# Kernel tuning notes

Measured on AMD Instinct MI355X. Metric: run time of the kernel, lower is better.

Reference implementation:

```python
import jax, jax.numpy as jnp
import numpy as np

SCALING = 32.0 / 16.0  # lora_alpha / lora_rank


def setup_inputs() -> dict:
    key = jax.random.key(0)
    ks = jax.random.split(key, 6)
    B_, S, D, O, E, R = 4, 2048, 4096, 4096, 8, 16
    x = jax.random.normal(ks[0], (B_, S, D), dtype=jnp.float32)
    W_base = jax.random.normal(ks[1], (O, D), dtype=jnp.float32) * (D ** -0.5)
    b_base = jax.random.normal(ks[2], (O,), dtype=jnp.float32) * 0.01
    W_gate = jax.random.normal(ks[3], (E, D), dtype=jnp.float32) * (D ** -0.5)
    A = jax.random.normal(ks[4], (E, R, D), dtype=jnp.float32) * (D ** -0.5)
    B = jax.random.normal(ks[5], (O, R), dtype=jnp.float32)[None] * (R ** -0.5)
    B = jnp.broadcast_to(B, (E, O, R)) * jnp.linspace(0.5, 1.5, E)[:, None, None]
    return {"x": x, "W_base": W_base, "b_base": b_base, "W_gate": W_gate,
            "A": A, "B": B, "top_k": 2}


def reference(x, W_base, b_base, W_gate, A, B, top_k):
    D = x.shape[-1]
    O = W_base.shape[0]
    E = W_gate.shape[0]
    xf = x.reshape(-1, D)                      # [N, D] flattened tokens
    N = xf.shape[0]

    # base linear
    base = jnp.einsum('nd,od->no', xf, W_base) + b_base          # [N, O]

    # gating: softmax then top-k, renormalize selected weights
    gate_logits = jax.nn.softmax(xf @ W_gate.T, axis=-1)          # [N, E]
    w, sel = jax.lax.top_k(gate_logits, top_k)                    # [N, k]
    w = w / jnp.sum(w, axis=-1, keepdims=True)

    # dense per-(token, expert) weight; non-selected experts get 0,
    # equivalent to the scatter-add combine in the original code.
    w_dense = jnp.zeros((N, E), dtype=x.dtype).at[
        jnp.arange(N)[:, None], sel].set(w)                       # [N, E]

    # LoRA expert compute: down-proj for every expert (rank is small),
    # weight, then up-proj and combine across experts.
    h = jnp.einsum('nd,erd->ner', xf, A)                          # [N, E, R]
    hw = h * w_dense[:, :, None]                                  # [N, E, R]
    moe = jnp.einsum('ner,eor->no', hw, B) * SCALING              # [N, O]

    out = (base + moe).reshape(x.shape[:-1] + (O,))
    return out
```

## Files before the change

### kernel.cpp

```cpp
#include <hip/hip_runtime.h>
#include <stdint.h>

typedef unsigned short u16;
typedef float f32x4 __attribute__((ext_vector_type(4)));
typedef short bf16x8 __attribute__((ext_vector_type(8)));

static __device__ __forceinline__ u16 f2bf(float f) {
  union { float f; unsigned u; } a; a.f = f;
  unsigned r = a.u + 0x7fffu + ((a.u >> 16) & 1u);
  return (u16)(r >> 16);
}

static __device__ __forceinline__ void gld16(const void* g, void* l) {
  __builtin_amdgcn_global_load_lds(
      (const __attribute__((address_space(1))) void*)(uintptr_t)g,
      (__attribute__((address_space(3))) void*)(uintptr_t)l,
      16, 0, 0);
}

__global__ __launch_bounds__(256, 4) void fused_pre(
    const float* __restrict__ x, const float* __restrict__ Wg,
    const float* __restrict__ Wb, const float* __restrict__ B,
    const float* __restrict__ A,
    u16* __restrict__ Xaug, u16* __restrict__ Waug, u16* __restrict__ a2,
    float* __restrict__ wsc) {
  const int bid = blockIdx.x;
  const int t = threadIdx.x;
  if (bid < 512) {
    const int lane = t & 63;
    const int wv = t >> 6;
    const int n0 = bid * 16 + wv * 4;
    const float4* g4 = (const float4*)Wg;
    float acc[4][8] = {};
#pragma unroll 2
    for (int ii = 0; ii < 16; ++ii) {
      const int i = ii * 64 + lane;
      float4 xv[4];
#pragma unroll
      for (int tok = 0; tok < 4; ++tok) {
        xv[tok] = *(const float4*)(x + (size_t)(n0 + tok) * 4096 + i * 4);
        ushort4 o;
        o.x = f2bf(xv[tok].x); o.y = f2bf(xv[tok].y);
        o.z = f2bf(xv[tok].z); o.w = f2bf(xv[tok].w);
        *(ushort4*)(Xaug + (size_t)(n0 + tok) * 4224 + i * 4) = o;
      }
#pragma unroll
      for (int e = 0; e < 8; ++e) {
        float4 w4 = g4[e * 1024 + i];
#pragma unroll
        for (int tok = 0; tok < 4; ++tok)
          acc[tok][e] += xv[tok].x * w4.x + xv[tok].y * w4.y +
                         xv[tok].z * w4.z + xv[tok].w * w4.w;
      }
    }
#pragma unroll
    for (int tok = 0; tok < 4; ++tok) {
#pragma unroll
      for (int e = 0; e < 8; ++e) {
#pragma unroll
        for (int off = 32; off > 0; off >>= 1)
          acc[tok][e] += __shfl_xor(acc[tok][e], off);
      }
      int i1 = 0; float m1 = acc[tok][0];
#pragma unroll
      for (int e = 1; e < 8; ++e) if (acc[tok][e] > m1) { m1 = acc[tok][e]; i1 = e; }
      int i2 = -1; float m2 = -3.4e38f;
#pragma unroll
      for (int e = 0; e < 8; ++e)
        if (e != i1 && acc[tok][e] > m2) { m2 = acc[tok][e]; i2 = e; }
      float w1 = 1.0f / (1.0f + expf(m2 - m1));
      float w2 = 1.0f - w1;
      if (lane < 8)
        wsc[(size_t)(n0 + tok) * 8 + lane] =
            (lane == i1) ? w1 : ((lane == i2) ? w2 : 0.0f);
    }
  } else if (bid < 2560) {
    const int total = 4096 * 1056;
    for (int v = (bid - 512) * 256 + t; v < total; v += 2048 * 256) {
      const int o = v / 1056;
      const int c = (v - o * 1056) * 4;
      ushort4 out;
      if (c < 4096) {
        float4 w = *(const float4*)(Wb + (size_t)o * 4096 + c);
        out.x = f2bf(w.x); out.y = f2bf(w.y); out.z = f2bf(w.z); out.w = f2bf(w.w);
      } else {
        const int er = c - 4096;
        const int e = er >> 4;
        const int r = er & 15;
        const float* bp = B + ((size_t)e * 4096 + o) * 16 + r;
        out.x = f2bf(bp[0] * 2.0f); out.y = f2bf(bp[1] * 2.0f);
        out.z = f2bf(bp[2] * 2.0f); out.w = f2bf(bp[3] * 2.0f);
      }
      *(ushort4*)(Waug + (size_t)o * 4224 + c) = out;
    }
  } else {
    const int i = (bid - 2560) * 256 + t;
    const size_t e = (size_t)i * 4;
    float4 v = *(const float4*)(A + e);
    ushort4 o;
    o.x = f2bf(v.x); o.y = f2bf(v.y); o.z = f2bf(v.z); o.w = f2bf(v.w);
    *(ushort4*)(a2 + e) = o;
  }
}

__global__ __launch_bounds__(256) void lora_hw(
    const u16* __restrict__ Xa, const u16* __restrict__ A2,
    const float* __restrict__ wsc, u16* __restrict__ Xaug) {
  __shared__ __align__(1024) char lds[40960];
  const int t = threadIdx.x;
  const int lane = t & 63;
  const int w = t >> 6;
  const int l15 = lane & 15, lhi = lane >> 4;
  const int brow = blockIdx.x * 32;

  const int sb = (lane << 4) ^ (lane & 32);
  const int srow = sb >> 6;
  const int scol = (sb & 63) >> 1;

  const u16* pA = Xa + (size_t)(brow + (w >> 1) * 16 + srow) * 4224 + (w & 1) * 32 + scol;
  const u16* pB[4];
#pragma unroll
  for (int s = 0; s < 4; ++s) {
    const int idx = w * 4 + s;
    pB[s] = A2 + (size_t)((idx >> 1) * 16 + srow) * 4096 + (idx & 1) * 32 + scol;
  }
  const int dA = w << 10;
  const int dB = 4096 + (w << 12);
  const int innerL = ((l15 << 6) + (lhi << 4)) ^ ((l15 & 8) << 2);

  f32x4 acc[2][2] = {};

  gld16(pA, lds + dA);
#pragma unroll
  for (int s = 0; s < 4; ++s) gld16(pB[s], lds + dB + (s << 10));

  for (int j = 0; j < 64; ++j) {
    const int buf = (j & 1) * 20480;
    const int obuf = buf ^ 20480;
    if (j < 63) {
      const int k1 = (j + 1) * 64;
      gld16(pA + k1, lds + obuf + dA);
#pragma unroll
      for (int s = 0; s < 4; ++s) gld16(pB[s] + k1, lds + obuf + dB + (s << 10));
      asm volatile("s_waitcnt vmcnt(5)" ::: "memory");
    } else {
      asm volatile("s_waitcnt vmcnt(0)" ::: "memory");
    }
    __syncthreads();
    bf16x8 av[2][2], bv[2][2];
#pragma unroll
    for (int m = 0; m < 2; ++m)
#pragma unroll
      for (int kk = 0; kk < 2; ++kk)
        av[m][kk] = *(const bf16x8*)(lds + buf + ((m * 2 + kk) << 10) + innerL);
#pragma unroll
    for (int n = 0; n < 2; ++n)
#pragma unroll
      for (int kk = 0; kk < 2; ++kk)
        bv[n][kk] = *(const bf16x8*)(lds + buf + 4096 + (((w * 2 + n) * 2 + kk) << 10) + innerL);
#pragma unroll
    for (int kk = 0; kk < 2; ++kk)
#pragma unroll
      for (int m = 0; m < 2; ++m)
#pragma unroll
        for (int n = 0; n < 2; ++n)
          acc[m][n] = __builtin_amdgcn_mfma_f32_16x16x32_bf16(av[m][kk], bv[n][kk], acc[m][n], 0, 0, 0);
    __syncthreads();
  }
#pragma unroll
  for (int m = 0; m < 2; ++m) {
    const int rbase = brow + m * 16 + lhi * 4;
#pragma unroll
    for (int n = 0; n < 2; ++n) {
      const int col = w * 32 + n * 16 + l15;
#pragma unroll
      for (int j = 0; j < 4; ++j) {
        const int row = rbase + j;
        const float g = wsc[(size_t)row * 8 + (col >> 4)];
        Xaug[(size_t)row * 4224 + 4096 + col] = f2bf(acc[m][n][j] * g);
      }
    }
  }
}

#define BAR do { asm volatile("" ::: "memory"); __builtin_amdgcn_s_barrier(); asm volatile("" ::: "memory"); } while (0)

#define RDA(BUF, MH)                                                            \
  { _Pragma("unroll") for (int mm = 0; mm < 4; ++mm)                            \
    _Pragma("unroll") for (int kk = 0; kk < 2; ++kk)                            \
      av[mm][kk] = *(const bf16x8*)(lds + (BUF) + fbA + ((((MH) * 4 + mm) * 2 + kk) << 10)); }

#define RDB(BUF, NH)                                                            \
  { _Pragma("unroll") for (int nn = 0; nn < 2; ++nn)                            \
    _Pragma("unroll") for (int kk = 0; kk < 2; ++kk)                            \
      bv[(NH) * 2 + nn][kk] = *(const bf16x8*)(lds + (BUF) + fbB + ((((NH) * 2 + nn) * 2 + kk) << 10)); }

#define MFMAQ(MH, NH)                                                           \
  { __builtin_amdgcn_s_setprio(1);                                              \
    _Pragma("unroll") for (int kk = 0; kk < 2; ++kk)                            \
    _Pragma("unroll") for (int mm = 0; mm < 4; ++mm)                            \
    _Pragma("unroll") for (int nn = 0; nn < 2; ++nn)                            \
      acc[(MH) * 4 + mm][(NH) * 2 + nn] = __builtin_amdgcn_mfma_f32_16x16x32_bf16( \
          av[mm][kk], bv[(NH) * 2 + nn][kk], acc[(MH) * 4 + mm][(NH) * 2 + nn], 0, 0, 0); \
    __builtin_amdgcn_s_setprio(0); }

__global__ __launch_bounds__(512, 2) void gemm8p(
    const u16* __restrict__ Ag, const u16* __restrict__ Bg,
    const float* __restrict__ bias, float* __restrict__ C,
    int lda, int ldb, int ldc, int K) {
  __shared__ __align__(1024) char lds[131072];
  const int t = threadIdx.x;
  const int lane = t & 63;
  const int w = t >> 6;
  const int wr = w >> 2, wc = w & 3;
  const int l15 = lane & 15, lhi = lane >> 4;

  const int bid = blockIdx.x;
  const int g = bid >> 3;
  const int tile_m = (bid & 7) * 4 + (g & 3);
  const int tile_n = g >> 2;
  const int brow = tile_m << 8;
  const int bcol = tile_n << 8;

  const int sb = (lane << 4) ^ (lane & 32);
  const int srow = sb >> 6;
  const int scol = (sb & 63) >> 1;

  const u16* pA[4]; const u16* pB[4];
#pragma unroll
  for (int s = 0; s < 4; ++s) {
    const int idx = w * 4 + s;
    const int rg = idx >> 1, cs = idx & 1;
    pA[s] = Ag + (size_t)(brow + rg * 16 + srow) * lda + cs * 32 + scol;
    pB[s] = Bg + (size_t)(bcol + rg * 16 + srow) * ldb + cs * 32 + scol;
  }
  const int ldsA = w << 12;
  const int ldsB = 32768 + (w << 12);

  const int innerL = ((l15 << 6) + (lhi << 4)) ^ ((l15 & 8) << 2);
  const int fbA = (wr << 14) + innerL;
  const int fbB = 32768 + (wc << 13) + innerL;

  f32x4 acc[8][4] = {};
  bf16x8 av[4][2], bv[4][2];

  const int NT = K >> 6;

#pragma unroll
  for (int s = 0; s < 4; ++s) gld16(pA[s], lds + ldsA + (s << 10));
#pragma unroll
  for (int s = 0; s < 4; ++s) gld16(pB[s], lds + ldsB + (s << 10));
#pragma unroll
  for (int s = 0; s < 4; ++s) gld16(pB[s] + 64, lds + 65536 + ldsB + (s << 10));
#pragma unroll
  for (int s = 0; s < 4; ++s) { pA[s] += 64; pB[s] += 128; }
  asm volatile("s_waitcnt vmcnt(4)" ::: "memory");
  BAR;
  RDA(0, 0); RDB(0, 0);

  for (int j = 0; j < NT; ++j) {
    const int buf  = (j & 1) << 16;
    const int obuf = buf ^ 65536;
    const bool stA = (j + 1 < NT);
    const bool stB = (j + 2 < NT);
    if (stA) { gld16(pA[0], lds + obuf + ldsA);
               gld16(pA[1], lds + obuf + ldsA + 1024); }
    MFMAQ(0, 0);
    RDB(buf, 1);
    BAR;
    if (stA) { gld16(pA[2], lds + obuf + ldsA + 2048);
               gld16(pA[3], lds + obuf + ldsA + 3072); }
    MFMAQ(0, 1);
    RDA(buf, 1);
    BAR;
    if (stB) { gld16(pB[0], lds + buf + ldsB);
               gld16(pB[1], lds + buf + ldsB + 1024); }
    MFMAQ(1, 1);
    BAR;
    if (stB) { gld16(pB[2], lds + buf + ldsB + 2048);
               gld16(pB[3], lds + buf + ldsB + 3072); }
    if (j < NT - 2)       { asm volatile("s_waitcnt vmcnt(4)" ::: "memory"); }
    else if (j == NT - 2) { asm volatile("s_waitcnt vmcnt(0)" ::: "memory"); }
    BAR;
    MFMAQ(1, 0);
    if (stA) { RDA(obuf, 0); RDB(obuf, 0); }
#pragma unroll
    for (int s = 0; s < 4; ++s) { pA[s] += 64; pB[s] += 64; }
  }

#pragma unroll
  for (int m = 0; m < 8; ++m) {
    const int row0 = brow + wr * 128 + m * 16 + lhi * 4;
#pragma unroll
    for (int n = 0; n < 4; ++n) {
      const int col = bcol + wc * 64 + n * 16 + l15;
      const float b2 = bias[col];
#pragma unroll
      for (int jj = 0; jj < 4; ++jj)
        C[(size_t)(row0 + jj) * ldc + col] = acc[m][n][jj] + b2;
    }
  }
}

extern "C" void kernel_launch(void* const* d_in, const int* in_sizes, int n_in,
                              void* d_out, int out_size, void* d_ws, size_t ws_size,
                              hipStream_t stream) {
  const float* x  = (const float*)d_in[0];
  const float* Wb = (const float*)d_in[1];
  const float* bb = (const float*)d_in[2];
  const float* Wg = (const float*)d_in[3];
  const float* A  = (const float*)d_in[4];
  const float* B  = (const float*)d_in[5];
  float* out = (float*)d_out;

  char* ws = (char*)d_ws;
  u16*   Xaug = (u16*)ws;
  u16*   Waug = (u16*)(ws + 69206016);
  u16*   a2   = (u16*)(ws + 69206016 + 34603008);
  float* wsc  = (float*)(ws + 69206016 + 34603008 + 1048576);

  fused_pre<<<3072, 256, 0, stream>>>(x, Wg, Wb, B, A, Xaug, Waug, a2, wsc);

  lora_hw<<<256, 256, 0, stream>>>(Xaug, a2, wsc, Xaug);

  gemm8p<<<512, 512, 0, stream>>>(Xaug, Waug, bb, out, 4224, 4224, 4096, 4224);
}
```

Measured before the change: 331.3 us.

## Restructure GEMM main loop into half-tile staged ping-pong with interleaved wave ownership

Reworks the bf16 GEMM so that each 256x256 tile is split into halves of 128 rows. Each wave now owns interleaved 64x32 sub-blocks across both halves instead of one contiguous 128x64 block. The main loop is unrolled by two K-steps with explicit ping-pong buffers, and global-to-LDS loads are staged per half between barrier-bracketed MFMA quadrants. The intent is finer-grained overlap of loads with MFMA work and lower LDS read pressure, at the cost of many more barriers per iteration and an assumption that the K-tile count is even.

```diff
diff --git a/kernel.cpp b/kernel.cpp
--- a/kernel.cpp
+++ b/kernel.cpp
@@ -185,23 +185,38 @@
 
 #define BAR do { asm volatile("" ::: "memory"); __builtin_amdgcn_s_barrier(); asm volatile("" ::: "memory"); } while (0)
 
-#define RDA(BUF, MH)                                                            \
+#define STG_A(KT, H, DB) do {                                                   \
+    gld16(pAst + (size_t)(H) * 128 * lda + (size_t)(KT) * 64,                   \
+          lds + (DB) + (H) * 16384 + dstOff);                                   \
+    gld16(pAst + (size_t)((H) * 128 + 64) * lda + (size_t)(KT) * 64,            \
+          lds + (DB) + (H) * 16384 + dstOff + 8192);                            \
+  } while (0)
+#define STG_B(KT, H, DB) do {                                                   \
+    gld16(pBst + (size_t)(H) * 128 * ldb + (size_t)(KT) * 64,                   \
+          lds + (DB) + 32768 + (H) * 16384 + dstOff);                           \
+    gld16(pBst + (size_t)((H) * 128 + 64) * ldb + (size_t)(KT) * 64,            \
+          lds + (DB) + 32768 + (H) * 16384 + dstOff + 8192);                    \
+  } while (0)
+
+#define RDA8(DB, MH)                                                            \
   { _Pragma("unroll") for (int mm = 0; mm < 4; ++mm)                            \
     _Pragma("unroll") for (int kk = 0; kk < 2; ++kk)                            \
-      av[mm][kk] = *(const bf16x8*)(lds + (BUF) + fbA + ((((MH) * 4 + mm) * 2 + kk) << 10)); }
-
-#define RDB(BUF, NH)                                                            \
+      av[mm][kk] = *(const bf16x8*)(lds + (DB) + (MH) * 16384 +                 \
+                    (((wr * 4 + mm) * 2 + kk) << 10) + innerL); }
+
+#define RDB4(DB, NH, BV)                                                        \
   { _Pragma("unroll") for (int nn = 0; nn < 2; ++nn)                            \
     _Pragma("unroll") for (int kk = 0; kk < 2; ++kk)                            \
-      bv[(NH) * 2 + nn][kk] = *(const bf16x8*)(lds + (BUF) + fbB + ((((NH) * 2 + nn) * 2 + kk) << 10)); }
-
-#define MFMAQ(MH, NH)                                                           \
+      BV[nn][kk] = *(const bf16x8*)(lds + (DB) + 32768 + (NH) * 16384 +         \
+                    (((wc * 2 + nn) * 2 + kk) << 10) + innerL); }
+
+#define MQ(MH, NH, BV)                                                          \
   { __builtin_amdgcn_s_setprio(1);                                              \
     _Pragma("unroll") for (int kk = 0; kk < 2; ++kk)                            \
     _Pragma("unroll") for (int mm = 0; mm < 4; ++mm)                            \
     _Pragma("unroll") for (int nn = 0; nn < 2; ++nn)                            \
       acc[(MH) * 4 + mm][(NH) * 2 + nn] = __builtin_amdgcn_mfma_f32_16x16x32_bf16( \
-          av[mm][kk], bv[(NH) * 2 + nn][kk], acc[(MH) * 4 + mm][(NH) * 2 + nn], 0, 0, 0); \
+          av[mm][kk], BV[nn][kk], acc[(MH) * 4 + mm][(NH) * 2 + nn], 0, 0, 0);  \
     __builtin_amdgcn_s_setprio(0); }
 
 __global__ __launch_bounds__(512, 2) void gemm8p(
@@ -223,81 +238,66 @@
   const int bcol = tile_n << 8;
 
   const int sb = (lane << 4) ^ (lane & 32);
-  const int srow = sb >> 6;
-  const int scol = (sb & 63) >> 1;
-
-  const u16* pA[4]; const u16* pB[4];
-#pragma unroll
-  for (int s = 0; s < 4; ++s) {
-    const int idx = w * 4 + s;
-    const int rg = idx >> 1, cs = idx & 1;
-    pA[s] = Ag + (size_t)(brow + rg * 16 + srow) * lda + cs * 32 + scol;
-    pB[s] = Bg + (size_t)(bcol + rg * 16 + srow) * ldb + cs * 32 + scol;
-  }
-  const int ldsA = w << 12;
-  const int ldsB = 32768 + (w << 12);
+  const int r0 = (w >> 1) * 16 + (sb >> 6);
+  const int c0 = (w & 1) * 32 + ((sb & 63) >> 1);
+  const u16* pAst = Ag + (size_t)(brow + r0) * lda + c0;
+  const u16* pBst = Bg + (size_t)(bcol + r0) * ldb + c0;
+  const int dstOff = w << 10;
 
   const int innerL = ((l15 << 6) + (lhi << 4)) ^ ((l15 & 8) << 2);
-  const int fbA = (wr << 14) + innerL;
-  const int fbB = 32768 + (wc << 13) + innerL;
 
   f32x4 acc[8][4] = {};
-  bf16x8 av[4][2], bv[4][2];
+  bf16x8 av[4][2], bv[2][2], bv2[2][2];
 
   const int NT = K >> 6;
-
-#pragma unroll
-  for (int s = 0; s < 4; ++s) gld16(pA[s], lds + ldsA + (s << 10));
-#pragma unroll
-  for (int s = 0; s < 4; ++s) gld16(pB[s], lds + ldsB + (s << 10));
-#pragma unroll
-  for (int s = 0; s < 4; ++s) gld16(pB[s] + 64, lds + 65536 + ldsB + (s << 10));
-#pragma unroll
-  for (int s = 0; s < 4; ++s) { pA[s] += 64; pB[s] += 128; }
+  const int NIT = NT >> 1;
+
+  STG_A(0, 0, 0); STG_A(0, 1, 0); STG_B(0, 0, 0); STG_B(0, 1, 0);
+  STG_B(1, 0, 65536); STG_A(1, 0, 65536);
   asm volatile("s_waitcnt vmcnt(4)" ::: "memory");
   BAR;
-  RDA(0, 0); RDB(0, 0);
-
-  for (int j = 0; j < NT; ++j) {
-    const int buf  = (j & 1) << 16;
-    const int obuf = buf ^ 65536;
-    const bool stA = (j + 1 < NT);
-    const bool stB = (j + 2 < NT);
-    if (stA) { gld16(pA[0], lds + obuf + ldsA);
-               gld16(pA[1], lds + obuf + ldsA + 1024); }
-    MFMAQ(0, 0);
-    RDB(buf, 1);
-    BAR;
-    if (stA) { gld16(pA[2], lds + obuf + ldsA + 2048);
-               gld16(pA[3], lds + obuf + ldsA + 3072); }
-    MFMAQ(0, 1);
-    RDA(buf, 1);
-    BAR;
-    if (stB) { gld16(pB[0], lds + buf + ldsB);
-               gld16(pB[1], lds + buf + ldsB + 1024); }
-    MFMAQ(1, 1);
-    BAR;
-    if (stB) { gld16(pB[2], lds + buf + ldsB + 2048);
-               gld16(pB[3], lds + buf + ldsB + 3072); }
-    if (j < NT - 2)       { asm volatile("s_waitcnt vmcnt(4)" ::: "memory"); }
-    else if (j == NT - 2) { asm volatile("s_waitcnt vmcnt(0)" ::: "memory"); }
-    BAR;
-    MFMAQ(1, 0);
-    if (stA) { RDA(obuf, 0); RDB(obuf, 0); }
-#pragma unroll
-    for (int s = 0; s < 4; ++s) { pA[s] += 64; pB[s] += 64; }
-  }
-
-#pragma unroll
-  for (int m = 0; m < 8; ++m) {
-    const int row0 = brow + wr * 128 + m * 16 + lhi * 4;
-#pragma unroll
-    for (int n = 0; n < 4; ++n) {
-      const int col = bcol + wc * 64 + n * 16 + l15;
+
+  for (int i = 0; i < NIT; ++i) {
+    const int e = 2 * i;
+    const int o = e + 1;
+    const bool st2 = (i + 1 < NIT);
+    RDA8(0, 0); RDB4(0, 0, bv);
+    STG_B(o, 1, 65536);
+    BAR; MQ(0, 0, bv); BAR;
+    RDB4(0, 1, bv2);
+    STG_A(o, 1, 65536);
+    BAR; MQ(0, 1, bv2); BAR;
+    RDA8(0, 1);
+    if (st2) STG_B(e + 2, 0, 0);
+    BAR; MQ(1, 1, bv2); BAR;
+    if (st2) STG_A(e + 2, 0, 0);
+    if (st2) { asm volatile("s_waitcnt vmcnt(4)" ::: "memory"); }
+    else     { asm volatile("s_waitcnt vmcnt(0)" ::: "memory"); }
+    BAR; MQ(1, 0, bv); BAR;
+    RDA8(65536, 0); RDB4(65536, 0, bv);
+    if (st2) STG_B(e + 2, 1, 0);
+    BAR; MQ(0, 0, bv); BAR;
+    RDB4(65536, 1, bv2);
+    if (st2) STG_A(e + 2, 1, 0);
+    BAR; MQ(0, 1, bv2); BAR;
+    RDA8(65536, 1);
+    if (st2) STG_B(o + 2, 0, 65536);
+    BAR; MQ(1, 1, bv2); BAR;
+    if (st2) STG_A(o + 2, 0, 65536);
+    asm volatile("s_waitcnt vmcnt(4)" ::: "memory");
+    BAR; MQ(1, 0, bv); BAR;
+  }
+
+#pragma unroll
+  for (int mi = 0; mi < 8; ++mi) {
+    const int row0 = brow + (mi >> 2) * 128 + wr * 64 + (mi & 3) * 16 + lhi * 4;
+#pragma unroll
+    for (int ni = 0; ni < 4; ++ni) {
+      const int col = bcol + (ni >> 1) * 128 + wc * 32 + (ni & 1) * 16 + l15;
       const float b2 = bias[col];
 #pragma unroll
       for (int jj = 0; jj < 4; ++jj)
-        C[(size_t)(row0 + jj) * ldc + col] = acc[m][n][jj] + b2;
+        C[(size_t)(row0 + jj) * ldc + col] = acc[mi][ni][jj] + b2;
     }
   }
 }
```

Result: slower. 338.9 us (+2.3%).
